# Kernel optimization log

Hardware: AMD Instinct MI355X
Metric: run time of the kernel (lower is better)

## Reference

```python
import jax, jax.numpy as jnp
import numpy as np

N_USER = 50000
N_ITEM = 50000
E = 500000
D = 256
H = 8
DK = D // H
EPS = 1e-5
SQRT_DK = float(np.sqrt(DK))


def _layernorm(x, g, b):
    m = jnp.mean(x, axis=-1, keepdims=True)
    v = jnp.var(x, axis=-1, keepdims=True)
    return (x - m) * jax.lax.rsqrt(v + EPS) * g + b


def _etype_aggregate(h_src, h_dst, src, dst, n_dst, Wk, bk, Wq, bq, Wv, bv, pri, att, msg):
    # per-ntype K/Q/V projections, then per-relation head-wise transforms
    k = (h_src @ Wk + bk).reshape(-1, H, DK)
    v = (h_src @ Wv + bv).reshape(-1, H, DK)
    q = (h_dst @ Wq + bq).reshape(-1, H, DK)
    k = jnp.einsum('nhi,hij->nhj', k, att)
    v = jnp.einsum('nhi,hij->nhj', v, msg)
    # v_dot_u score per edge per head: [E, H]
    score = jnp.einsum('ehd,ehd->eh', q[dst], k[src]) * pri / SQRT_DK
    # edge_softmax normalized per destination node (per head)
    smax = jax.ops.segment_max(score, dst, num_segments=n_dst)
    ex = jnp.exp(score - smax[dst])
    ssum = jax.ops.segment_sum(ex, dst, num_segments=n_dst)
    a = ex / ssum[dst]
    # u_mul_e + sum reduce (zero-in-degree dst nodes get zeros, like DGL sum)
    t = jax.ops.segment_sum(v[src] * a[:, :, None], dst, num_segments=n_dst)
    return t.reshape(n_dst, D)


def _dst_update(t, h, Wa, ba, skip, g, b):
    alpha = jax.nn.sigmoid(skip)
    out = (t @ Wa + ba) * alpha + h * (1.0 - alpha)
    return _layernorm(out, g, b)


def _forward(h_user, h_item, src_ui, dst_ui, src_iu, dst_iu, Wk_user, bk_user, Wq_user, bq_user, Wv_user, bv_user, Wa_user, ba_user, ln_g_user, ln_b_user, skip_user, Wk_item, bk_item, Wq_item, bq_item, Wv_item, bv_item, Wa_item, ba_item, ln_g_item, ln_b_item, skip_item, pri_ui, att_ui, msg_ui, pri_iu, att_iu, msg_iu):
    # (user, click, item): k/v from src ntype 'user', q from dst ntype 'item'
    t_item = _etype_aggregate(h_user, h_item, src_ui, dst_ui, N_ITEM, Wk_user, bk_user, Wq_item, bq_item, Wv_user, bv_user, pri_ui, att_ui, msg_ui)
    # (item, rev_click, user)
    t_user = _etype_aggregate(h_item, h_user, src_iu, dst_iu, N_USER, Wk_item, bk_item, Wq_user, bq_user, Wv_item, bv_item, pri_iu, att_iu, msg_iu)
    # each ntype is dst of exactly one etype -> cross_reducer 'mean' is identity
    new_user = _dst_update(t_user, h_user, Wa_user, ba_user, skip_user, ln_g_user, ln_b_user)
    new_item = _dst_update(t_item, h_item, Wa_item, ba_item, skip_item, ln_g_item, ln_b_item)
    return jnp.stack([new_user, new_item])  # [2, N, D]


def setup_inputs() -> dict:
    key = jax.random.key(0)
    ks = jax.random.split(key, 16)

    def xavier(k, shape):
        s = np.sqrt(2.0 / (shape[-2] + shape[-1]))
        return (jax.random.normal(k, shape, dtype=jnp.float32) * s).astype(jnp.float32)

    inp = {}
    inp['h_user'] = jax.random.normal(ks[0], (N_USER, D), dtype=jnp.float32)
    inp['h_item'] = jax.random.normal(ks[1], (N_ITEM, D), dtype=jnp.float32)
    inp['src_ui'] = jax.random.randint(ks[2], (E,), 0, N_USER, dtype=jnp.int32)
    inp['dst_ui'] = jax.random.randint(ks[3], (E,), 0, N_ITEM, dtype=jnp.int32)
    inp['src_iu'] = jax.random.randint(ks[4], (E,), 0, N_ITEM, dtype=jnp.int32)
    inp['dst_iu'] = jax.random.randint(ks[5], (E,), 0, N_USER, dtype=jnp.int32)
    i = 6
    for nt in ['user', 'item']:
        for nm in ['k', 'q', 'v', 'a']:
            inp[f'W{nm}_{nt}'] = xavier(jax.random.fold_in(ks[i], hash(nm) % 1000), (D, D))
            inp[f'b{nm}_{nt}'] = jnp.zeros((D,), jnp.float32)
        i += 1
        inp[f'ln_g_{nt}'] = jnp.ones((D,), jnp.float32)
        inp[f'ln_b_{nt}'] = jnp.zeros((D,), jnp.float32)
        inp[f'skip_{nt}'] = jnp.ones((1,), jnp.float32)
    for et in ['ui', 'iu']:
        inp[f'pri_{et}'] = jnp.ones((H,), jnp.float32)
        inp[f'att_{et}'] = xavier(ks[i], (H, DK, DK)); i += 1
        inp[f'msg_{et}'] = xavier(ks[i], (H, DK, DK)); i += 1
    return inp


def reference(h_user, h_item, src_ui, dst_ui, src_iu, dst_iu, Wk_user, bk_user, Wq_user, bq_user, Wv_user, bv_user, Wa_user, ba_user, ln_g_user, ln_b_user, skip_user, Wk_item, bk_item, Wq_item, bq_item, Wv_item, bv_item, Wa_item, ba_item, ln_g_item, ln_b_item, skip_item, pri_ui, att_ui, msg_ui, pri_iu, att_iu, msg_iu):
    return _forward(h_user, h_item, src_ui, dst_ui, src_iu, dst_iu, Wk_user, bk_user, Wq_user, bq_user, Wv_user, bv_user, Wa_user, ba_user, ln_g_user, ln_b_user, skip_user, Wk_item, bk_item, Wq_item, bq_item, Wv_item, bv_item, Wa_item, ba_item, ln_g_item, ln_b_item, skip_item, pri_ui, att_ui, msg_ui, pri_iu, att_iu, msg_iu)
```

## Files before the change

kernel.cpp:

```cpp
#include <hip/hip_runtime.h>

#define NN 50000
#define DD 256
#define HH 8
#define EE 500000
#define INV_SQRT_DK 0.17677669529663687f

typedef __attribute__((ext_vector_type(8))) short bf16x8;
typedef __attribute__((ext_vector_type(4))) float f32x4;

__device__ __forceinline__ unsigned short f2bf(float f) {
    unsigned int u = __float_as_uint(f);
    u = (u + 0x7FFFu + ((u >> 16) & 1u)) >> 16;
    return (unsigned short)u;
}
__device__ __forceinline__ float bf2f(unsigned short u) {
    return __uint_as_float(((unsigned int)u) << 16);
}
__device__ __forceinline__ float bflo(unsigned int u) {
    return __uint_as_float(u << 16);
}
__device__ __forceinline__ float bfhi(unsigned int u) {
    return __uint_as_float(u & 0xFFFF0000u);
}

__global__ __launch_bounds__(256) void conv_bf16(const float* __restrict__ Xu,
                                                 const float* __restrict__ Xi,
                                                 unsigned short* __restrict__ Yu,
                                                 unsigned short* __restrict__ Yi) {
    const size_t ND = (size_t)NN * DD;
    size_t i = ((size_t)blockIdx.x * 256 + threadIdx.x) * 4;
    const float* X = Xu; unsigned short* Y = Yu;
    if (i >= ND) { X = Xi; Y = Yi; i -= ND; }
    float4 v = *(const float4*)&X[i];
    ushort4 o;
    o.x = f2bf(v.x); o.y = f2bf(v.y); o.z = f2bf(v.z); o.w = f2bf(v.w);
    *(ushort4*)&Y[i] = o;
}

__global__ __launch_bounds__(256) void fuse_kernel(const float* __restrict__ Wk_u, const float* __restrict__ bk_u,
                                                   const float* __restrict__ att_ui_,
                                                   const float* __restrict__ Wv_u, const float* __restrict__ bv_u,
                                                   const float* __restrict__ msg_ui_,
                                                   const float* __restrict__ Wk_i, const float* __restrict__ bk_i,
                                                   const float* __restrict__ att_iu_,
                                                   const float* __restrict__ Wv_i, const float* __restrict__ bv_i,
                                                   const float* __restrict__ msg_iu_,
                                                   unsigned short* __restrict__ BTu, float* __restrict__ beffU,
                                                   unsigned short* __restrict__ BTi, float* __restrict__ beffI) {
    int y = blockIdx.y;
    const float* W = (y == 0) ? Wk_u : (y == 1) ? Wv_u : (y == 2) ? Wk_i : Wv_i;
    const float* b = (y == 0) ? bk_u : (y == 1) ? bv_u : (y == 2) ? bk_i : bv_i;
    const float* T = (y == 0) ? att_ui_ : (y == 1) ? msg_ui_ : (y == 2) ? att_iu_ : msg_iu_;
    unsigned short* WT = (y < 2) ? BTu : BTi;
    float* be = (y < 2) ? beffU : beffI;
    int j = threadIdx.x;
    int h = j >> 5, jj = j & 31;
    int pj = ((j >> 2) << 3) + (j & 3) + ((y & 1) ? 4 : 0);
    const float* Th = T + h * 1024;
    if (blockIdx.x < 256) {
        int c = blockIdx.x;
        float acc = 0.f;
        #pragma unroll 8
        for (int i = 0; i < 32; ++i) acc += W[c * 256 + h * 32 + i] * Th[i * 32 + jj];
        WT[pj * 256 + c] = f2bf(acc);
    } else {
        float acc = 0.f;
        #pragma unroll 8
        for (int i = 0; i < 32; ++i) acc += b[h * 32 + i] * Th[i * 32 + jj];
        be[pj] = acc;
    }
}

__global__ __launch_bounds__(256) void convT_kernel(const float* __restrict__ Wq_u, const float* __restrict__ bq_u,
                                                    const float* __restrict__ Wq_i, const float* __restrict__ bq_i,
                                                    const float* __restrict__ Wa_u, const float* __restrict__ Wa_i,
                                                    unsigned short* __restrict__ BTu, float* __restrict__ beffU,
                                                    unsigned short* __restrict__ BTi, float* __restrict__ beffI,
                                                    unsigned short* __restrict__ WaTu, unsigned short* __restrict__ WaTi) {
    int y = blockIdx.y;
    const float* W = (y == 0) ? Wq_u : (y == 1) ? Wq_i : (y == 2) ? Wa_u : Wa_i;
    unsigned short* WT = (y == 0) ? BTu + 512 * 256 : (y == 1) ? BTi + 512 * 256 : (y == 2) ? WaTu : WaTi;
    int k = blockIdx.x, n = threadIdx.x;
    WT[n * 256 + k] = f2bf(W[k * 256 + n]);
    if (k == 0 && y < 2) {
        float* be = (y == 0) ? beffU : beffI;
        const float* bq = (y == 0) ? bq_u : bq_i;
        be[512 + n] = bq[n];
    }
}

__global__ void hist_kernel(const int* __restrict__ dst_ui, const int* __restrict__ dst_iu,
                            int* __restrict__ cnt) {
    int e = blockIdx.x * blockDim.x + threadIdx.x;
    if (e < EE) atomicAdd(&cnt[dst_ui[e]], 1);
    else if (e < 2 * EE) atomicAdd(&cnt[NN + dst_iu[e - EE]], 1);
}

__global__ __launch_bounds__(256) void alloc_kernel(const int* __restrict__ cnt,
                                                    int* __restrict__ start,
                                                    int* __restrict__ ctr) {
    int y = blockIdx.y;
    int i = blockIdx.x * 256 + threadIdx.x;
    int idx = y * NN + i;
    int v = (i < NN) ? cnt[idx] : 0;
    int lane = threadIdx.x & 63;
    int pre = v;
    #pragma unroll
    for (int o = 1; o < 64; o <<= 1) {
        int u = __shfl_up(pre, o, 64);
        if (lane >= o) pre += u;
    }
    int wsum = __shfl(pre, 63, 64);
    int base = 0;
    if (lane == 63) base = atomicAdd(&ctr[y], wsum);
    base = __shfl(base, 63, 64);
    if (i < NN) start[idx] = y * EE + base + pre - v;
}

__global__ void scatter_kernel(const int* __restrict__ dst_ui, const int* __restrict__ src_ui,
                               const int* __restrict__ dst_iu, const int* __restrict__ src_iu,
                               const int* __restrict__ start, int* __restrict__ cur,
                               int* __restrict__ srcid) {
    int e = blockIdx.x * blockDim.x + threadIdx.x;
    int d, s;
    if (e < EE) { d = dst_ui[e]; s = src_ui[e]; }
    else if (e < 2 * EE) { d = NN + dst_iu[e - EE]; s = src_iu[e - EE]; }
    else return;
    int pos = start[d] + atomicAdd(&cur[d], 1);
    srcid[pos] = s;
}

__global__ __launch_bounds__(256) void gemm_kvq(const unsigned short* __restrict__ Au,
                                                const unsigned short* __restrict__ Ai,
                                                const unsigned short* __restrict__ BTu,
                                                const unsigned short* __restrict__ BTi,
                                                const float* __restrict__ beffU,
                                                const float* __restrict__ beffI,
                                                unsigned short* __restrict__ KVu,
                                                unsigned short* __restrict__ KVi,
                                                unsigned short* __restrict__ Qu,
                                                unsigned short* __restrict__ Qi) {
    __shared__ __align__(16) char smem[20480];
    bf16x8* As = (bf16x8*)smem;
    bf16x8* Bs = (bf16x8*)(smem + 10240);
    int z = blockIdx.z;
    const unsigned short* A = z ? Ai : Au;
    const unsigned short* BT = z ? BTi : BTu;
    const float* beff = z ? beffI : beffU;
    unsigned short* KV = z ? KVi : KVu;
    unsigned short* Qb = z ? Qi : Qu;
    int bm = blockIdx.x * 128, bn = blockIdx.y * 128;
    int tid = threadIdx.x;
    int lane = tid & 63, w = tid >> 6;
    int wm = (w & 1) * 64, wn = (w >> 1) * 64;
    int m16 = lane & 15, q = lane >> 4;
    f32x4 acc[4][4] = {};
    for (int k0 = 0; k0 < 256; k0 += 32) {
        #pragma unroll
        for (int cc = 0; cc < 2; ++cc) {
            int c = tid + cc * 256;
            int row = c >> 2, off8 = c & 3;
            int gr = bm + row;
            bf16x8 va = {};
            if (gr < NN) va = *(const bf16x8*)&A[(size_t)gr * 256 + k0 + off8 * 8];
            As[row * 5 + off8] = va;
            Bs[row * 5 + off8] = *(const bf16x8*)&BT[(size_t)(bn + row) * 256 + k0 + off8 * 8];
        }
        __syncthreads();
        bf16x8 af[4], bfr[4];
        #pragma unroll
        for (int i = 0; i < 4; ++i) af[i] = As[(wm + 16 * i + m16) * 5 + q];
        #pragma unroll
        for (int j = 0; j < 4; ++j) bfr[j] = Bs[(wn + 16 * j + m16) * 5 + q];
        #pragma unroll
        for (int i = 0; i < 4; ++i)
            #pragma unroll
            for (int j = 0; j < 4; ++j)
                acc[i][j] = __builtin_amdgcn_mfma_f32_16x16x32_bf16(af[i], bfr[j], acc[i][j], 0, 0, 0);
        __syncthreads();
    }
    const bool isKV = (bn < 512);
    unsigned short* dstb = isKV ? KV : Qb;
    const int rowlen = isKV ? 512 : 256;
    const int coloff = isKV ? bn : (bn - 512);
    unsigned short* Cs = (unsigned short*)smem;
    #pragma unroll
    for (int half = 0; half < 2; ++half) {
        if ((w & 1) == half) {
            #pragma unroll
            for (int i = 0; i < 4; ++i) {
                int rloc = 16 * i + q * 4;
                #pragma unroll
                for (int j = 0; j < 4; ++j) {
                    int cl = wn + 16 * j + m16;
                    float bv = beff[bn + cl];
                    #pragma unroll
                    for (int r = 0; r < 4; ++r)
                        Cs[(rloc + r) * 136 + cl] = f2bf(acc[i][j][r] + bv);
                }
            }
        }
        __syncthreads();
        #pragma unroll
        for (int it = 0; it < 4; ++it) {
            int idx = it * 256 + tid;
            int row = idx >> 4, seg = idx & 15;
            int gr = bm + half * 64 + row;
            if (gr < NN) {
                bf16x8 v = *(const bf16x8*)&Cs[row * 136 + seg * 8];
                *(bf16x8*)&dstb[(size_t)gr * rowlen + coloff + seg * 8] = v;
            }
        }
        __syncthreads();
    }
}

__global__ __launch_bounds__(256) void gemm_out(const unsigned short* __restrict__ A0,
                                                const unsigned short* __restrict__ A1,
                                                const unsigned short* __restrict__ BT0,
                                                const unsigned short* __restrict__ BT1,
                                                const float* __restrict__ bias0,
                                                const float* __restrict__ bias1,
                                                float* __restrict__ C0,
                                                float* __restrict__ C1) {
    __shared__ bf16x8 As[128 * 5];
    __shared__ bf16x8 Bs[128 * 5];
    int z = blockIdx.z;
    const unsigned short* A = z ? A1 : A0;
    const unsigned short* BT = z ? BT1 : BT0;
    const float* bias = z ? bias1 : bias0;
    float* C = z ? C1 : C0;
    int bm = blockIdx.x * 128, bn = blockIdx.y * 128;
    int tid = threadIdx.x;
    int lane = tid & 63, w = tid >> 6;
    int wm = (w & 1) * 64, wn = (w >> 1) * 64;
    int m16 = lane & 15, q = lane >> 4;
    f32x4 acc[4][4] = {};
    for (int k0 = 0; k0 < 256; k0 += 32) {
        #pragma unroll
        for (int cc = 0; cc < 2; ++cc) {
            int c = tid + cc * 256;
            int row = c >> 2, off8 = c & 3;
            int gr = bm + row;
            bf16x8 va = {};
            if (gr < NN) va = *(const bf16x8*)&A[(size_t)gr * 256 + k0 + off8 * 8];
            As[row * 5 + off8] = va;
            Bs[row * 5 + off8] = *(const bf16x8*)&BT[(size_t)(bn + row) * 256 + k0 + off8 * 8];
        }
        __syncthreads();
        bf16x8 af[4], bfr[4];
        #pragma unroll
        for (int i = 0; i < 4; ++i) af[i] = As[(wm + 16 * i + m16) * 5 + q];
        #pragma unroll
        for (int j = 0; j < 4; ++j) bfr[j] = Bs[(wn + 16 * j + m16) * 5 + q];
        #pragma unroll
        for (int i = 0; i < 4; ++i)
            #pragma unroll
            for (int j = 0; j < 4; ++j)
                acc[i][j] = __builtin_amdgcn_mfma_f32_16x16x32_bf16(af[i], bfr[j], acc[i][j], 0, 0, 0);
        __syncthreads();
    }
    #pragma unroll
    for (int i = 0; i < 4; ++i) {
        int rb = bm + wm + 16 * i + q * 4;
        #pragma unroll
        for (int j = 0; j < 4; ++j) {
            int col = bn + wn + 16 * j + m16;
            float bv = bias[col];
            #pragma unroll
            for (int r = 0; r < 4; ++r) {
                int row = rb + r;
                if (row < NN) C[(size_t)row * 256 + col] = acc[i][j][r] + bv;
            }
        }
    }
}

__global__ __launch_bounds__(256) void fused_agg(const int* __restrict__ start,
                                                 const int* __restrict__ cnt,
                                                 const int* __restrict__ srcid,
                                                 const unsigned short* __restrict__ Qi,
                                                 const unsigned short* __restrict__ Qu,
                                                 const unsigned short* __restrict__ KVu,
                                                 const unsigned short* __restrict__ KVi,
                                                 const float* __restrict__ pri_ui,
                                                 const float* __restrict__ pri_iu,
                                                 unsigned short* __restrict__ tI16,
                                                 unsigned short* __restrict__ tU16) {
    int w = threadIdx.x >> 6;
    int lane = threadIdx.x & 63;
    int b = blockIdx.x * 4 + w;
    bool second = (b >= NN);
    int d = second ? b - NN : b;
    const unsigned short* Q = second ? Qu : Qi;
    const unsigned short* KV = second ? KVi : KVu;
    const float* pri = second ? pri_iu : pri_ui;
    unsigned short* T = second ? tU16 : tI16;

    int h = lane >> 3;
    float sscale = pri[h] * INV_SQRT_DK;
    ushort4 q4 = *(const ushort4*)&Q[(size_t)d * 256 + lane * 4];
    float qx = bf2f(q4.x), qy = bf2f(q4.y), qz = bf2f(q4.z), qw = bf2f(q4.w);

    int p0 = start[b], n = cnt[b];
    float a0 = 0.f, a1 = 0.f, a2 = 0.f, a3 = 0.f, l = 0.f;

#define LDKV(idx) (*(const uint4*)&KV[(size_t)__shfl(myS, (idx), 64) * 512 + lane * 8])
#define PROC(kv) { \
        float sc = qx * bflo(kv.x) + qy * bfhi(kv.x) + qz * bflo(kv.y) + qw * bfhi(kv.y); \
        sc += __shfl_xor(sc, 1, 8); \
        sc += __shfl_xor(sc, 2, 8); \
        sc += __shfl_xor(sc, 4, 8); \
        float wgt = __expf(sc * sscale); \
        a0 += wgt * bflo(kv.z); \
        a1 += wgt * bfhi(kv.z); \
        a2 += wgt * bflo(kv.w); \
        a3 += wgt * bfhi(kv.w); \
        l += wgt; }

    for (int base = 0; base < n; base += 64) {
        int rem = n - base; if (rem > 64) rem = 64;
        int myS = (lane < rem) ? srcid[p0 + base + lane] : 0;
        uint4 k0 = {}, k1 = {}, k2 = {}, k3 = {};
        if (0 < rem) k0 = LDKV(0);
        if (1 < rem) k1 = LDKV(1);
        if (2 < rem) k2 = LDKV(2);
        if (3 < rem) k3 = LDKV(3);
        int t = 0;
        for (; t + 4 <= rem; t += 4) {
            PROC(k0); if (t + 4 < rem) k0 = LDKV(t + 4);
            PROC(k1); if (t + 5 < rem) k1 = LDKV(t + 5);
            PROC(k2); if (t + 6 < rem) k2 = LDKV(t + 6);
            PROC(k3); if (t + 7 < rem) k3 = LDKV(t + 7);
        }
        if (t < rem)     PROC(k0);
        if (t + 1 < rem) PROC(k1);
        if (t + 2 < rem) PROC(k2);
    }
#undef LDKV
#undef PROC

    float inv = (l > 0.f) ? 1.f / l : 0.f;
    ushort4 o;
    o.x = f2bf(a0 * inv); o.y = f2bf(a1 * inv);
    o.z = f2bf(a2 * inv); o.w = f2bf(a3 * inv);
    *(ushort4*)&T[(size_t)d * 256 + lane * 4] = o;
}

__global__ __launch_bounds__(256) void update_kernel(const float* __restrict__ tmpU,
                                                     const float* __restrict__ tmpI,
                                                     const float* __restrict__ hU,
                                                     const float* __restrict__ hI,
                                                     const float* __restrict__ skipU,
                                                     const float* __restrict__ skipI,
                                                     const float* __restrict__ gU, const float* __restrict__ bU,
                                                     const float* __restrict__ gI, const float* __restrict__ bI,
                                                     float* __restrict__ out) {
    int w = threadIdx.x >> 6;
    int lane = threadIdx.x & 63;
    int b = blockIdx.x * 4 + w;
    bool second = (b >= NN);
    int row = second ? b - NN : b;
    const float* tmp = second ? tmpI : tmpU;
    const float* hb = second ? hI : hU;
    const float* skp = second ? skipI : skipU;
    const float* g = second ? gI : gU;
    const float* bb = second ? bI : bU;
    float* o = out + (second ? (size_t)NN * DD : 0);

    float alpha = 1.f / (1.f + __expf(-skp[0]));
    float4 tm = *(const float4*)&tmp[(size_t)row * 256 + lane * 4];
    float4 hh = *(const float4*)&hb[(size_t)row * 256 + lane * 4];
    float x0 = tm.x * alpha + hh.x * (1.f - alpha);
    float x1 = tm.y * alpha + hh.y * (1.f - alpha);
    float x2 = tm.z * alpha + hh.z * (1.f - alpha);
    float x3 = tm.w * alpha + hh.w * (1.f - alpha);
    float s = x0 + x1 + x2 + x3;
    #pragma unroll
    for (int off = 32; off > 0; off >>= 1) s += __shfl_xor(s, off, 64);
    float mean = s * (1.f / 256.f);
    float d0 = x0 - mean, d1 = x1 - mean, d2 = x2 - mean, d3 = x3 - mean;
    float s2 = d0 * d0 + d1 * d1 + d2 * d2 + d3 * d3;
    #pragma unroll
    for (int off = 32; off > 0; off >>= 1) s2 += __shfl_xor(s2, off, 64);
    float rstd = rsqrtf(s2 * (1.f / 256.f) + 1e-5f);
    float4 g4 = *(const float4*)&g[lane * 4];
    float4 b4 = *(const float4*)&bb[lane * 4];
    float4 r;
    r.x = d0 * rstd * g4.x + b4.x;
    r.y = d1 * rstd * g4.y + b4.y;
    r.z = d2 * rstd * g4.z + b4.z;
    r.w = d3 * rstd * g4.w + b4.w;
    *(float4*)&o[(size_t)row * 256 + lane * 4] = r;
}

extern "C" void kernel_launch(void* const* d_in, const int* in_sizes, int n_in,
                              void* d_out, int out_size, void* d_ws, size_t ws_size,
                              hipStream_t stream) {
    const float* h_user  = (const float*)d_in[0];
    const float* h_item  = (const float*)d_in[1];
    const int*   src_ui  = (const int*)d_in[2];
    const int*   dst_ui  = (const int*)d_in[3];
    const int*   src_iu  = (const int*)d_in[4];
    const int*   dst_iu  = (const int*)d_in[5];
    const float* Wk_user = (const float*)d_in[6];
    const float* bk_user = (const float*)d_in[7];
    const float* Wq_user = (const float*)d_in[8];
    const float* bq_user = (const float*)d_in[9];
    const float* Wv_user = (const float*)d_in[10];
    const float* bv_user = (const float*)d_in[11];
    const float* Wa_user = (const float*)d_in[12];
    const float* ba_user = (const float*)d_in[13];
    const float* ln_g_user = (const float*)d_in[14];
    const float* ln_b_user = (const float*)d_in[15];
    const float* skip_user = (const float*)d_in[16];
    const float* Wk_item = (const float*)d_in[17];
    const float* bk_item = (const float*)d_in[18];
    const float* Wq_item = (const float*)d_in[19];
    const float* bq_item = (const float*)d_in[20];
    const float* Wv_item = (const float*)d_in[21];
    const float* bv_item = (const float*)d_in[22];
    const float* Wa_item = (const float*)d_in[23];
    const float* ba_item = (const float*)d_in[24];
    const float* ln_g_item = (const float*)d_in[25];
    const float* ln_b_item = (const float*)d_in[26];
    const float* skip_item = (const float*)d_in[27];
    const float* pri_ui = (const float*)d_in[28];
    const float* att_ui = (const float*)d_in[29];
    const float* msg_ui = (const float*)d_in[30];
    const float* pri_iu = (const float*)d_in[31];
    const float* att_iu = (const float*)d_in[32];
    const float* msg_iu = (const float*)d_in[33];
    float* out = (float*)d_out;

    const size_t ND = (size_t)NN * DD;

    unsigned short* up = (unsigned short*)d_ws;
    unsigned short* KVu = up;  up += (size_t)NN * 512;
    unsigned short* KVi = up;  up += (size_t)NN * 512;
    unsigned short* Qu  = up;  up += ND;
    unsigned short* Qi  = up;  up += ND;
    unsigned short* hU16 = up; up += ND;
    unsigned short* hI16 = up; up += ND;
    unsigned short* BTu = up;  up += 768 * 256;
    unsigned short* BTi = up;  up += 768 * 256;
    unsigned short* WaTu = up; up += 65536;
    unsigned short* WaTi = up; up += 65536;
    float* fp = (float*)up;
    float* beffU = fp; fp += 768;
    float* beffI = fp; fp += 768;
    int* ip = (int*)fp;
    int* cnt   = ip; ip += 2 * NN;
    int* cur   = ip; ip += 2 * NN;
    int* ctr   = ip; ip += 2;
    int* start = ip; ip += 2 * NN;
    int* srcid = ip; ip += 2 * EE;
    unsigned short* tU16 = hU16;
    unsigned short* tI16 = hI16;
    float* projU = (float*)KVu;
    float* projI = (float*)KVi;

    const int eb = (EE + 255) / 256;

    conv_bf16<<<2 * 12500, 256, 0, stream>>>(h_user, h_item, hU16, hI16);
    fuse_kernel<<<dim3(257, 4), 256, 0, stream>>>(Wk_user, bk_user, att_ui, Wv_user, bv_user, msg_ui,
                                                  Wk_item, bk_item, att_iu, Wv_item, bv_item, msg_iu,
                                                  BTu, beffU, BTi, beffI);
    convT_kernel<<<dim3(256, 4), 256, 0, stream>>>(Wq_user, bq_user, Wq_item, bq_item, Wa_user, Wa_item,
                                                   BTu, beffU, BTi, beffI, WaTu, WaTi);
    hipMemsetAsync(cnt, 0, (4 * NN + 2) * sizeof(int), stream);
    hist_kernel<<<2 * eb, 256, 0, stream>>>(dst_ui, dst_iu, cnt);
    alloc_kernel<<<dim3(196, 2), 256, 0, stream>>>(cnt, start, ctr);
    scatter_kernel<<<2 * eb, 256, 0, stream>>>(dst_ui, src_ui, dst_iu, src_iu, start, cur, srcid);

    gemm_kvq<<<dim3(391, 6, 2), 256, 0, stream>>>(hU16, hI16, BTu, BTi, beffU, beffI,
                                                  KVu, KVi, Qu, Qi);

    fused_agg<<<25000, 256, 0, stream>>>(start, cnt, srcid, Qi, Qu, KVu, KVi,
                                         pri_ui, pri_iu, tI16, tU16);

    gemm_out<<<dim3(391, 2, 2), 256, 0, stream>>>(tU16, tI16, WaTu, WaTi, ba_user, ba_item,
                                                  projU, projI);
    update_kernel<<<25000, 256, 0, stream>>>(projU, projI, h_user, h_item,
                                             skip_user, skip_item,
                                             ln_g_user, ln_b_user, ln_g_item, ln_b_item, out);
}
```

Before: 712.5 us.

## Fuse output projection GEMM with skip-blend and LayerNorm epilogue

Replaces the separate output GEMM and update/LayerNorm kernel with one kernel. Each 512-thread block computes a full 128x256 row tile, so full rows are available for LayerNorm. The fp32 accumulators are staged through shared memory in 32-row chunks, and the bias, sigmoid skip blend and LayerNorm are applied before writing the output. This removes the write and re-read of the fp32 projection intermediate and one kernel launch. In exchange, the grid shrinks to 782 blocks with more shared memory per block, and the epilogue adds extra barriers.

```diff
diff --git a/kernel.cpp b/kernel.cpp
--- a/kernel.cpp
+++ b/kernel.cpp
@@ -216,64 +216,110 @@
     }
 }
 
-__global__ __launch_bounds__(256) void gemm_out(const unsigned short* __restrict__ A0,
-                                                const unsigned short* __restrict__ A1,
-                                                const unsigned short* __restrict__ BT0,
-                                                const unsigned short* __restrict__ BT1,
-                                                const float* __restrict__ bias0,
-                                                const float* __restrict__ bias1,
-                                                float* __restrict__ C0,
-                                                float* __restrict__ C1) {
-    __shared__ bf16x8 As[128 * 5];
-    __shared__ bf16x8 Bs[128 * 5];
-    int z = blockIdx.z;
+__global__ __launch_bounds__(512) void gemm_ln(const unsigned short* __restrict__ A0,
+                                               const unsigned short* __restrict__ A1,
+                                               const unsigned short* __restrict__ BT0,
+                                               const unsigned short* __restrict__ BT1,
+                                               const float* __restrict__ ba0,
+                                               const float* __restrict__ ba1,
+                                               const float* __restrict__ h0,
+                                               const float* __restrict__ h1,
+                                               const float* __restrict__ skp0,
+                                               const float* __restrict__ skp1,
+                                               const float* __restrict__ g0, const float* __restrict__ be0,
+                                               const float* __restrict__ g1, const float* __restrict__ be1,
+                                               float* __restrict__ out) {
+    __shared__ __align__(16) char smem[33280];
+    bf16x8* As = (bf16x8*)smem;
+    bf16x8* Bs = (bf16x8*)(smem + 10240);
+    float* Es = (float*)smem;
+    int z = blockIdx.y;
     const unsigned short* A = z ? A1 : A0;
     const unsigned short* BT = z ? BT1 : BT0;
-    const float* bias = z ? bias1 : bias0;
-    float* C = z ? C1 : C0;
-    int bm = blockIdx.x * 128, bn = blockIdx.y * 128;
+    const float* ba = z ? ba1 : ba0;
+    const float* hb = z ? h1 : h0;
+    const float* skp = z ? skp1 : skp0;
+    const float* g = z ? g1 : g0;
+    const float* bb = z ? be1 : be0;
+    float* o = out + (z ? (size_t)NN * DD : 0);
+
+    int bm = blockIdx.x * 128;
     int tid = threadIdx.x;
     int lane = tid & 63, w = tid >> 6;
-    int wm = (w & 1) * 64, wn = (w >> 1) * 64;
     int m16 = lane & 15, q = lane >> 4;
-    f32x4 acc[4][4] = {};
+    f32x4 acc[16] = {};
     for (int k0 = 0; k0 < 256; k0 += 32) {
-        #pragma unroll
-        for (int cc = 0; cc < 2; ++cc) {
-            int c = tid + cc * 256;
-            int row = c >> 2, off8 = c & 3;
+        {
+            int row = tid >> 2, ch = tid & 3;
             int gr = bm + row;
             bf16x8 va = {};
-            if (gr < NN) va = *(const bf16x8*)&A[(size_t)gr * 256 + k0 + off8 * 8];
-            As[row * 5 + off8] = va;
-            Bs[row * 5 + off8] = *(const bf16x8*)&BT[(size_t)(bn + row) * 256 + k0 + off8 * 8];
-        }
-        __syncthreads();
-        bf16x8 af[4], bfr[4];
-        #pragma unroll
-        for (int i = 0; i < 4; ++i) af[i] = As[(wm + 16 * i + m16) * 5 + q];
-        #pragma unroll
-        for (int j = 0; j < 4; ++j) bfr[j] = Bs[(wn + 16 * j + m16) * 5 + q];
-        #pragma unroll
-        for (int i = 0; i < 4; ++i)
+            if (gr < NN) va = *(const bf16x8*)&A[(size_t)gr * 256 + k0 + ch * 8];
+            As[row * 5 + ch] = va;
+        }
+        #pragma unroll
+        for (int cc = 0; cc < 2; ++cc) {
+            int idx = tid + cc * 512;
+            int n = idx >> 2, ch = idx & 3;
+            Bs[n * 5 + ch] = *(const bf16x8*)&BT[(size_t)n * 256 + k0 + ch * 8];
+        }
+        __syncthreads();
+        bf16x8 af = As[(w * 16 + m16) * 5 + q];
+        #pragma unroll
+        for (int jh = 0; jh < 2; ++jh) {
+            bf16x8 bfr[8];
             #pragma unroll
-            for (int j = 0; j < 4; ++j)
-                acc[i][j] = __builtin_amdgcn_mfma_f32_16x16x32_bf16(af[i], bfr[j], acc[i][j], 0, 0, 0);
-        __syncthreads();
-    }
+            for (int jj = 0; jj < 8; ++jj) bfr[jj] = Bs[((jh * 8 + jj) * 16 + m16) * 5 + q];
+            #pragma unroll
+            for (int jj = 0; jj < 8; ++jj)
+                acc[jh * 8 + jj] = __builtin_amdgcn_mfma_f32_16x16x32_bf16(af, bfr[jj], acc[jh * 8 + jj], 0, 0, 0);
+        }
+        __syncthreads();
+    }
+    float alpha = 1.f / (1.f + __expf(-skp[0]));
+    float am1 = 1.f - alpha;
+    float4 ba4 = *(const float4*)&ba[lane * 4];
+    float4 g4 = *(const float4*)&g[lane * 4];
+    float4 b4 = *(const float4*)&bb[lane * 4];
     #pragma unroll
-    for (int i = 0; i < 4; ++i) {
-        int rb = bm + wm + 16 * i + q * 4;
-        #pragma unroll
-        for (int j = 0; j < 4; ++j) {
-            int col = bn + wn + 16 * j + m16;
-            float bv = bias[col];
+    for (int p = 0; p < 4; ++p) {
+        if ((w >> 1) == p) {
+            int rbase = (w & 1) * 16 + 4 * q;
             #pragma unroll
-            for (int r = 0; r < 4; ++r) {
-                int row = rb + r;
-                if (row < NN) C[(size_t)row * 256 + col] = acc[i][j][r] + bv;
+            for (int j = 0; j < 16; ++j)
+                #pragma unroll
+                for (int rr = 0; rr < 4; ++rr)
+                    Es[(rbase + rr) * 260 + 16 * j + m16] = acc[j][rr];
+        }
+        __syncthreads();
+        #pragma unroll
+        for (int rrr = 0; rrr < 4; ++rrr) {
+            int lrow = w * 4 + rrr;
+            int gr = bm + 32 * p + lrow;
+            if (gr < NN) {
+                float4 tm = *(const float4*)&Es[lrow * 260 + lane * 4];
+                float4 hh = *(const float4*)&hb[(size_t)gr * 256 + lane * 4];
+                float x0 = (tm.x + ba4.x) * alpha + hh.x * am1;
+                float x1 = (tm.y + ba4.y) * alpha + hh.y * am1;
+                float x2 = (tm.z + ba4.z) * alpha + hh.z * am1;
+                float x3 = (tm.w + ba4.w) * alpha + hh.w * am1;
+                float s = x0 + x1 + x2 + x3;
+                #pragma unroll
+                for (int off = 32; off > 0; off >>= 1) s += __shfl_xor(s, off, 64);
+                float mean = s * (1.f / 256.f);
+                float d0 = x0 - mean, d1 = x1 - mean, d2 = x2 - mean, d3 = x3 - mean;
+                float s2 = d0 * d0 + d1 * d1 + d2 * d2 + d3 * d3;
+                #pragma unroll
+                for (int off = 32; off > 0; off >>= 1) s2 += __shfl_xor(s2, off, 64);
+                float rstd = rsqrtf(s2 * (1.f / 256.f) + 1e-5f);
+                float4 r;
+                r.x = d0 * rstd * g4.x + b4.x;
+                r.y = d1 * rstd * g4.y + b4.y;
+                r.z = d2 * rstd * g4.z + b4.z;
+                r.w = d3 * rstd * g4.w + b4.w;
+                *(float4*)&o[(size_t)gr * 256 + lane * 4] = r;
             }
         }
+        __syncthreads();
     }
 }
 
@@ -346,53 +392,6 @@
     o.x = f2bf(a0 * inv); o.y = f2bf(a1 * inv);
     o.z = f2bf(a2 * inv); o.w = f2bf(a3 * inv);
     *(ushort4*)&T[(size_t)d * 256 + lane * 4] = o;
-}
-
-__global__ __launch_bounds__(256) void update_kernel(const float* __restrict__ tmpU,
-                                                     const float* __restrict__ tmpI,
-                                                     const float* __restrict__ hU,
-                                                     const float* __restrict__ hI,
-                                                     const float* __restrict__ skipU,
-                                                     const float* __restrict__ skipI,
-                                                     const float* __restrict__ gU, const float* __restrict__ bU,
-                                                     const float* __restrict__ gI, const float* __restrict__ bI,
-                                                     float* __restrict__ out) {
-    int w = threadIdx.x >> 6;
-    int lane = threadIdx.x & 63;
-    int b = blockIdx.x * 4 + w;
-    bool second = (b >= NN);
-    int row = second ? b - NN : b;
-    const float* tmp = second ? tmpI : tmpU;
-    const float* hb = second ? hI : hU;
-    const float* skp = second ? skipI : skipU;
-    const float* g = second ? gI : gU;
-    const float* bb = second ? bI : bU;
-    float* o = out + (second ? (size_t)NN * DD : 0);
-
-    float alpha = 1.f / (1.f + __expf(-skp[0]));
-    float4 tm = *(const float4*)&tmp[(size_t)row * 256 + lane * 4];
-    float4 hh = *(const float4*)&hb[(size_t)row * 256 + lane * 4];
-    float x0 = tm.x * alpha + hh.x * (1.f - alpha);
-    float x1 = tm.y * alpha + hh.y * (1.f - alpha);
-    float x2 = tm.z * alpha + hh.z * (1.f - alpha);
-    float x3 = tm.w * alpha + hh.w * (1.f - alpha);
-    float s = x0 + x1 + x2 + x3;
-    #pragma unroll
-    for (int off = 32; off > 0; off >>= 1) s += __shfl_xor(s, off, 64);
-    float mean = s * (1.f / 256.f);
-    float d0 = x0 - mean, d1 = x1 - mean, d2 = x2 - mean, d3 = x3 - mean;
-    float s2 = d0 * d0 + d1 * d1 + d2 * d2 + d3 * d3;
-    #pragma unroll
-    for (int off = 32; off > 0; off >>= 1) s2 += __shfl_xor(s2, off, 64);
-    float rstd = rsqrtf(s2 * (1.f / 256.f) + 1e-5f);
-    float4 g4 = *(const float4*)&g[lane * 4];
-    float4 b4 = *(const float4*)&bb[lane * 4];
-    float4 r;
-    r.x = d0 * rstd * g4.x + b4.x;
-    r.y = d1 * rstd * g4.y + b4.y;
-    r.z = d2 * rstd * g4.z + b4.z;
-    r.w = d3 * rstd * g4.w + b4.w;
-    *(float4*)&o[(size_t)row * 256 + lane * 4] = r;
 }
 
 extern "C" void kernel_launch(void* const* d_in, const int* in_sizes, int n_in,
@@ -458,8 +457,6 @@
     int* srcid = ip; ip += 2 * EE;
     unsigned short* tU16 = hU16;
     unsigned short* tI16 = hI16;
-    float* projU = (float*)KVu;
-    float* projI = (float*)KVi;
 
     const int eb = (EE + 255) / 256;
 
@@ -480,9 +477,7 @@
     fused_agg<<<25000, 256, 0, stream>>>(start, cnt, srcid, Qi, Qu, KVu, KVi,
                                          pri_ui, pri_iu, tI16, tU16);
 
-    gemm_out<<<dim3(391, 2, 2), 256, 0, stream>>>(tU16, tI16, WaTu, WaTi, ba_user, ba_item,
-                                                  projU, projI);
-    update_kernel<<<25000, 256, 0, stream>>>(projU, projI, h_user, h_item,
-                                             skip_user, skip_item,
-                                             ln_g_user, ln_b_user, ln_g_item, ln_b_item, out);
-}
+    gemm_ln<<<dim3(391, 2), 512, 0, stream>>>(tU16, tI16, WaTu, WaTi, ba_user, ba_item,
+                                              h_user, h_item, skip_user, skip_item,
+                                              ln_g_user, ln_b_user, ln_g_item, ln_b_item, out);
+}
```

Result: faster. 693.9 us (-2.6%).
